# Optimization experiments

Measured on AMD Instinct MI355X. Metric: run time of the kernel, lower is better.

Reference implementation:

```python
import jax, jax.numpy as jnp
import numpy as np

N, M, P, H = 200000, 20, 64, 256
EPS = 1e-12  # inside sqrt: avoids NaN grads when duplicate neighbors give zero distance


def setup_inputs() -> dict:
    key = jax.random.key(0)
    ks = jax.random.split(key, 8)
    x = jax.random.normal(ks[0], (N, P), jnp.float32)
    pos = jax.random.uniform(ks[1], (N, 2), jnp.float32) * 10.0
    y = jax.random.normal(ks[2], (N,), jnp.float32)
    # m distinct-from-self neighbor indices per node (offset trick avoids self loops)
    off = jax.random.randint(ks[3], (N, M), 1, N)
    nbr_idx = ((jnp.arange(N)[:, None] + off) % N).astype(jnp.int32)
    theta = jnp.array([1.0, 1.0, 0.1], jnp.float32)  # (sigma_sq, phi, tau)
    w1 = jax.random.normal(ks[4], (P, H), jnp.float32) * (1.0 / np.sqrt(P))
    b1 = jnp.zeros((H,), jnp.float32)
    w2 = jax.random.normal(ks[5], (H, 1), jnp.float32) * (1.0 / np.sqrt(H))
    b2 = jnp.zeros((1,), jnp.float32)
    return dict(x=x, pos=pos, y=y, nbr_idx=nbr_idx, theta=theta,
                w1=w1, b1=b1, w2=w2, b2=b2)


def _dist(a, b):
    return jnp.sqrt(jnp.sum((a - b) ** 2, axis=-1) + EPS)


def reference(x, pos, y, nbr_idx, theta, w1, b1, w2, b2):
    sigma_sq, phi, tau = theta[0], theta[1], theta[2]
    tau_sq = tau * sigma_sq
    m = nbr_idx.shape[1]
    pos_nbr = pos[nbr_idx]                                            # [N,M,2] gather
    # Cov(i, N(i)): exponential covariance of node-to-neighbor distances  [N,M]
    cov_i_ni = sigma_sq * jnp.exp(-phi * _dist(pos[:, None, :], pos_nbr))
    # Cov(N(i), N(i)) + nugget on the diagonal                          [N,M,M]
    d_nn = _dist(pos_nbr[:, :, None, :], pos_nbr[:, None, :, :])
    cov = sigma_sq * jnp.exp(-phi * d_nn) + tau_sq * jnp.eye(m, dtype=pos.dtype)
    # B_i = Cov(N,N)^{-1} Cov(i,N)  (batched small solve == inv @ vec)  [N,M]
    b_i = jnp.linalg.solve(cov, cov_i_ni[..., None])[..., 0]
    f_i = sigma_sq + tau - jnp.sum(b_i * cov_i_ni, axis=1)             # [N]
    inv_sqrt_f = 1.0 / jnp.sqrt(f_i)
    # MLP: Linear -> ReLU -> Linear, squeezed to [N]
    o = (jax.nn.relu(x @ w1 + b1) @ w2 + b2)[:, 0]
    y_decor = (y - jnp.sum(y[nbr_idx] * b_i, axis=1)) * inv_sqrt_f
    o_decor = (o - jnp.sum(o[nbr_idx] * b_i, axis=1)) * inv_sqrt_f
    return (y_decor, o_decor, o)
```

## Files before the change

kernel.cpp:

```cpp
#include <hip/hip_runtime.h>


#define MM   20
#define PP   64
#define HH   256
#define EPSF 1e-12f
#define UT(r, c) ((r)*21 - ((r)*((r)-1))/2 + ((c)-(r)))

typedef __attribute__((ext_vector_type(8))) short bf16x8;
typedef __attribute__((ext_vector_type(4))) float f32x4;

static __device__ __forceinline__ unsigned short f2bf(float f) {
    unsigned int u = __builtin_bit_cast(unsigned int, f);
    u += 0x7fffu + ((u >> 16) & 1u);
    return (unsigned short)(u >> 16);
}
static __device__ __forceinline__ float bf2f(unsigned short h) {
    unsigned int u = ((unsigned int)h) << 16;
    return __builtin_bit_cast(float, u);
}

__global__ __launch_bounds__(256, 2)
void mlp_mfma_kernel(const float* __restrict__ x,
                     const float* __restrict__ w1,
                     const float* __restrict__ b1,
                     const float* __restrict__ w2,
                     const float* __restrict__ b2,
                     float* __restrict__ o_out, int n)
{
    __shared__ __align__(16) short swh[PP * HH];
    __shared__ __align__(16) short swl[PP * HH];
    const int tid = threadIdx.x;

    {
        const int col = tid;
        const int t = col >> 4, nn = col & 15;
        #pragma unroll
        for (int g = 0; g < 8; ++g) {
            const int s = g >> 2, q = g & 3;
            bf16x8 hv, lv;
            #pragma unroll
            for (int u = 0; u < 8; ++u) {
                float v = w1[(g * 8 + u) * HH + col];
                unsigned short h = f2bf(v);
                hv[u] = (short)h;
                lv[u] = (short)f2bf(v - bf2f(h));
            }
            const int base = ((((t * 2 + s) * 4 + q) * 16) + nn) * 8;
            *(bf16x8*)&swh[base] = hv;
            *(bf16x8*)&swl[base] = lv;
        }
    }
    __syncthreads();

    const int lane = tid & 63;
    const int wv   = tid >> 6;
    const int nn   = lane & 15;
    const int q    = lane >> 4;
    const int wb   = blockIdx.x * 256 + wv * 64;

    float w2v[16], b1v[16];
    #pragma unroll
    for (int t = 0; t < 16; ++t) {
        w2v[t] = w2[t * 16 + nn];
        b1v[t] = b1[t * 16 + nn];
    }

    bf16x8 ah[4][2], al[4][2];
    #pragma unroll
    for (int mt = 0; mt < 4; ++mt) {
        const int row = wb + mt * 16 + nn;
        #pragma unroll
        for (int s = 0; s < 2; ++s) {
            float v[8];
            if (row < n) {
                const float* xp = x + (size_t)row * PP + s * 32 + q * 8;
                float4 va = *(const float4*)(xp);
                float4 vb = *(const float4*)(xp + 4);
                v[0]=va.x; v[1]=va.y; v[2]=va.z; v[3]=va.w;
                v[4]=vb.x; v[5]=vb.y; v[6]=vb.z; v[7]=vb.w;
            } else {
                #pragma unroll
                for (int u = 0; u < 8; ++u) v[u] = 0.0f;
            }
            bf16x8 h, l;
            #pragma unroll
            for (int u = 0; u < 8; ++u) {
                unsigned short hb = f2bf(v[u]);
                h[u] = (short)hb;
                l[u] = (short)f2bf(v[u] - bf2f(hb));
            }
            ah[mt][s] = h;
            al[mt][s] = l;
        }
    }

    float part[4][4];
    #pragma unroll
    for (int mt = 0; mt < 4; ++mt)
        #pragma unroll
        for (int r = 0; r < 4; ++r) part[mt][r] = 0.0f;

    for (int t = 0; t < 16; ++t) {
        f32x4 acc[4];
        #pragma unroll
        for (int mt = 0; mt < 4; ++mt) acc[mt] = (f32x4)(0.0f);
        #pragma unroll
        for (int s = 0; s < 2; ++s) {
            const int fb = ((((t * 2 + s) * 4 + q) * 16) + nn) * 8;
            bf16x8 bh = *(const bf16x8*)&swh[fb];
            bf16x8 bl = *(const bf16x8*)&swl[fb];
            #pragma unroll
            for (int mt = 0; mt < 4; ++mt) {
                acc[mt] = __builtin_amdgcn_mfma_f32_16x16x32_bf16(ah[mt][s], bh, acc[mt], 0, 0, 0);
                acc[mt] = __builtin_amdgcn_mfma_f32_16x16x32_bf16(al[mt][s], bh, acc[mt], 0, 0, 0);
                acc[mt] = __builtin_amdgcn_mfma_f32_16x16x32_bf16(ah[mt][s], bl, acc[mt], 0, 0, 0);
            }
        }
        #pragma unroll
        for (int mt = 0; mt < 4; ++mt)
            #pragma unroll
            for (int r = 0; r < 4; ++r)
                part[mt][r] = fmaf(fmaxf(acc[mt][r] + b1v[t], 0.0f), w2v[t], part[mt][r]);
    }

    #pragma unroll
    for (int w = 1; w < 16; w <<= 1)
        #pragma unroll
        for (int mt = 0; mt < 4; ++mt)
            #pragma unroll
            for (int r = 0; r < 4; ++r)
                part[mt][r] += __shfl_xor(part[mt][r], w, 64);

    const float bb = b2[0];
    if (nn == 0) {
        #pragma unroll
        for (int mt = 0; mt < 4; ++mt) {
            const int row = wb + mt * 16 + q * 4;
            if (row < n) {
                float4 o4 = make_float4(part[mt][0] + bb, part[mt][1] + bb,
                                        part[mt][2] + bb, part[mt][3] + bb);
                *(float4*)&o_out[row] = o4;
            }
        }
    }
}

__global__ __launch_bounds__(64, 1)
void solve_kernel(const float* __restrict__ pos,
                  const float* __restrict__ y,
                  const int*   __restrict__ nbr,
                  const float* __restrict__ theta,
                  const float* __restrict__ o_in,
                  float* __restrict__ yd,
                  float* __restrict__ od, int n)
{
    const int i = blockIdx.x * 64 + threadIdx.x;
    if (i >= n) return;

    const float sigma_sq = theta[0];
    const float phi      = theta[1];
    const float tau      = theta[2];
    const float tau_sq   = tau * sigma_sq;

    const float L2E = 1.44269504088896340736f;
    const float c1  = -phi * L2E;
    const float c0  = __builtin_amdgcn_logf(sigma_sq);

    int idx[MM];
    const int4* nb4 = (const int4*)(nbr + (size_t)i * MM);
    #pragma unroll
    for (int k = 0; k < MM / 4; ++k) {
        int4 v = nb4[k];
        idx[4*k] = v.x; idx[4*k+1] = v.y; idx[4*k+2] = v.z; idx[4*k+3] = v.w;
    }

    float px[21], py[21];
    const float2* pos2 = (const float2*)pos;
    #pragma unroll
    for (int j = 0; j < MM; ++j) {
        float2 p = pos2[idx[j]];
        px[j] = p.x; py[j] = p.y;
    }
    {
        float2 p = pos2[i];
        px[20] = p.x; py[20] = p.y;
    }

    const float sqrtEPS = __builtin_amdgcn_sqrtf(EPSF);
    const float diagA   = __builtin_amdgcn_exp2f(fmaf(sqrtEPS, c1, c0)) + tau_sq;

    float a[231];
    #pragma unroll
    for (int r = 0; r < 21; ++r) {
        #pragma unroll
        for (int c = r; c < 21; ++c) {
            if (r == c) {
                a[UT(r, c)] = (r == 20) ? (sigma_sq + tau) : diagA;
            } else {
                float dx = px[r] - px[c];
                float dy = py[r] - py[c];
                float d2 = fmaf(dx, dx, fmaf(dy, dy, EPSF));
                float d  = __builtin_amdgcn_sqrtf(d2);
                a[UT(r, c)] = __builtin_amdgcn_exp2f(fmaf(d, c1, c0));
            }
        }
    }

    float yv[21], ov[21];
    #pragma unroll
    for (int j = 0; j < MM; ++j) {
        yv[j] = y[idx[j]];
        ov[j] = o_in[idx[j]];
    }
    yv[20] = y[i];
    ov[20] = o_in[i];

    float pr[21], pd, pyv, pov;
    #pragma unroll 1
    for (int k = 0; k < 20; ++k) {
        switch (k) {
#define CASE(K) case K: {                                     \
            pd = a[UT(K, K)]; pyv = yv[K]; pov = ov[K];       \
            _Pragma("unroll")                                 \
            for (int c = K; c < 21; ++c) pr[c] = a[UT(K, c)]; \
        } break;
        CASE(0)  CASE(1)  CASE(2)  CASE(3)  CASE(4)
        CASE(5)  CASE(6)  CASE(7)  CASE(8)  CASE(9)
        CASE(10) CASE(11) CASE(12) CASE(13) CASE(14)
        CASE(15) CASE(16) CASE(17) CASE(18) CASE(19)
#undef CASE
        default: break;
        }
        float rp = __builtin_amdgcn_rcpf(pd);
        rp = rp * (2.0f - pd * rp);
        float m[21];
        #pragma unroll
        for (int r = 0; r < 21; ++r) {
            float mr = pr[r] * rp;
            m[r] = (r > k) ? mr : 0.0f;
        }
        #pragma unroll
        for (int r = 0; r < 21; ++r) {
            #pragma unroll
            for (int c = r; c < 21; ++c)
                a[UT(r, c)] = fmaf(-m[r], pr[c], a[UT(r, c)]);
            yv[r] = fmaf(-m[r], pyv, yv[r]);
            ov[r] = fmaf(-m[r], pov, ov[r]);
        }
    }

    const float f = a[UT(20, 20)];
    float is = __builtin_amdgcn_rsqf(f);
    is = is * fmaf(-0.5f * f * is, is, 1.5f);
    yd[i] = yv[20] * is;
    od[i] = ov[20] * is;
}

extern "C" void kernel_launch(void* const* d_in, const int* in_sizes, int n_in,
                              void* d_out, int out_size, void* d_ws, size_t ws_size,
                              hipStream_t stream)
{
    const float* x     = (const float*)d_in[0];
    const float* pos   = (const float*)d_in[1];
    const float* y     = (const float*)d_in[2];
    const int*   nbr   = (const int*)  d_in[3];
    const float* theta = (const float*)d_in[4];
    const float* w1    = (const float*)d_in[5];
    const float* b1    = (const float*)d_in[6];
    const float* w2    = (const float*)d_in[7];
    const float* b2    = (const float*)d_in[8];

    const int n = in_sizes[2];
    float* out = (float*)d_out;
    float* yd = out;
    float* od = out + (size_t)n;
    float* oo = out + 2 * (size_t)n;

    mlp_mfma_kernel<<<(n + 255) / 256, 256, 0, stream>>>(x, w1, b1, w2, b2, oo, n);
    solve_kernel<<<(n + 63) / 64, 64, 0, stream>>>(pos, y, nbr, theta, oo, yd, od, n);
}
```

Baseline: 234.2 us.

## Split each node's Gaussian elimination across lane pairs with column-interleaved storage

The solve kernel now gives each node to two adjacent lanes. Each lane holds the even or odd columns of the upper-triangular matrix, and one lane carries the y right-hand side while the other carries the o right-hand side. Pivots and multipliers are swapped between the pair with shuffles. This roughly halves the per-thread register array and lets the elimination loop be fully unrolled instead of dispatching through a switch, which aims to cut register pressure and raise occupancy (launch bounds now allow 2 blocks). The cost is extra shuffles, duplicated distance work for the shared column, and twice as many threads. The MLP kernel's outer loop over t is also unrolled.

```diff
diff --git a/kernel.cpp b/kernel.cpp
--- a/kernel.cpp
+++ b/kernel.cpp
@@ -5,7 +5,10 @@
 #define PP   64
 #define HH   256
 #define EPSF 1e-12f
-#define UT(r, c) ((r)*21 - ((r)*((r)-1))/2 + ((c)-(r)))
+
+#define QH(r)     ((r) >> 1)
+#define AIDX(r)   (11*(r) - (QH(r)*(QH(r)-1) + ((r)&1)*QH(r)))
+#define AT(r, s)  aL[AIDX(r) + (s) - QH(r)]
 
 typedef __attribute__((ext_vector_type(8))) short bf16x8;
 typedef __attribute__((ext_vector_type(4))) float f32x4;
@@ -101,6 +104,7 @@
         #pragma unroll
         for (int r = 0; r < 4; ++r) part[mt][r] = 0.0f;
 
+    #pragma unroll
     for (int t = 0; t < 16; ++t) {
         f32x4 acc[4];
         #pragma unroll
@@ -146,7 +150,7 @@
     }
 }
 
-__global__ __launch_bounds__(64, 1)
+__global__ __launch_bounds__(64, 2)
 void solve_kernel(const float* __restrict__ pos,
                   const float* __restrict__ y,
                   const int*   __restrict__ nbr,
@@ -155,7 +159,9 @@
                   float* __restrict__ yd,
                   float* __restrict__ od, int n)
 {
-    const int i = blockIdx.x * 64 + threadIdx.x;
+    const int lane = threadIdx.x;
+    const int h_   = lane & 1;
+    const int i    = blockIdx.x * 32 + (lane >> 1);
     if (i >= n) return;
 
     const float sigma_sq = theta[0];
@@ -167,6 +173,10 @@
     const float c1  = -phi * L2E;
     const float c0  = __builtin_amdgcn_logf(sigma_sq);
 
+    const float sqrtEPS = __builtin_amdgcn_sqrtf(EPSF);
+    const float diagA   = __builtin_amdgcn_exp2f(fmaf(sqrtEPS, c1, c0)) + tau_sq;
+    const float diagB   = sigma_sq + tau;
+
     int idx[MM];
     const int4* nb4 = (const int4*)(nbr + (size_t)i * MM);
     #pragma unroll
@@ -187,74 +197,76 @@
         px[20] = p.x; py[20] = p.y;
     }
 
-    const float sqrtEPS = __builtin_amdgcn_sqrtf(EPSF);
-    const float diagA   = __builtin_amdgcn_exp2f(fmaf(sqrtEPS, c1, c0)) + tau_sq;
-
-    float a[231];
-    #pragma unroll
-    for (int r = 0; r < 21; ++r) {
-        #pragma unroll
-        for (int c = r; c < 21; ++c) {
-            if (r == c) {
-                a[UT(r, c)] = (r == 20) ? (sigma_sq + tau) : diagA;
-            } else {
-                float dx = px[r] - px[c];
-                float dy = py[r] - py[c];
-                float d2 = fmaf(dx, dx, fmaf(dy, dy, EPSF));
-                float d  = __builtin_amdgcn_sqrtf(d2);
-                a[UT(r, c)] = __builtin_amdgcn_exp2f(fmaf(d, c1, c0));
-            }
-        }
-    }
-
-    float yv[21], ov[21];
-    #pragma unroll
-    for (int j = 0; j < MM; ++j) {
-        yv[j] = y[idx[j]];
-        ov[j] = o_in[idx[j]];
-    }
-    yv[20] = y[i];
-    ov[20] = o_in[i];
-
-    float pr[21], pd, pyv, pov;
-    #pragma unroll 1
+    float pxc[11], pyc[11];
+    #pragma unroll
+    for (int s = 0; s < 10; ++s) {
+        pxc[s] = h_ ? px[2*s+1] : px[2*s];
+        pyc[s] = h_ ? py[2*s+1] : py[2*s];
+    }
+    pxc[10] = px[20];
+    pyc[10] = py[20];
+
+    float bv[21];
+    {
+        const float* src = h_ ? o_in : y;
+        #pragma unroll
+        for (int j = 0; j < MM; ++j) bv[j] = src[idx[j]];
+        bv[20] = src[i];
+    }
+
+    float aL[131];
+    #pragma unroll
+    for (int r = 0; r <= 20; ++r) {
+        #pragma unroll
+        for (int s = QH(r); s <= 10; ++s) {
+            float dx = px[r] - pxc[s];
+            float dy = py[r] - pyc[s];
+            float d  = __builtin_amdgcn_sqrtf(fmaf(dx, dx, fmaf(dy, dy, EPSF)));
+            float v  = __builtin_amdgcn_exp2f(fmaf(d, c1, c0));
+            if (s == QH(r)) {
+                const float dv = (r == 20) ? diagB : diagA;
+                v = (h_ == (r & 1)) ? dv : v;
+            }
+            AT(r, s) = v;
+        }
+    }
+
+    #pragma unroll
     for (int k = 0; k < 20; ++k) {
-        switch (k) {
-#define CASE(K) case K: {                                     \
-            pd = a[UT(K, K)]; pyv = yv[K]; pov = ov[K];       \
-            _Pragma("unroll")                                 \
-            for (int c = K; c < 21; ++c) pr[c] = a[UT(K, c)]; \
-        } break;
-        CASE(0)  CASE(1)  CASE(2)  CASE(3)  CASE(4)
-        CASE(5)  CASE(6)  CASE(7)  CASE(8)  CASE(9)
-        CASE(10) CASE(11) CASE(12) CASE(13) CASE(14)
-        CASE(15) CASE(16) CASE(17) CASE(18) CASE(19)
-#undef CASE
-        default: break;
-        }
+        float sendv = AT(k, QH(k));
+        float recvv = __shfl_xor(sendv, 1, 64);
+        float pd = ((k & 1) == h_) ? sendv : recvv;
         float rp = __builtin_amdgcn_rcpf(pd);
         rp = rp * (2.0f - pd * rp);
-        float m[21];
-        #pragma unroll
-        for (int r = 0; r < 21; ++r) {
-            float mr = pr[r] * rp;
-            m[r] = (r > k) ? mr : 0.0f;
-        }
-        #pragma unroll
-        for (int r = 0; r < 21; ++r) {
-            #pragma unroll
-            for (int c = r; c < 21; ++c)
-                a[UT(r, c)] = fmaf(-m[r], pr[c], a[UT(r, c)]);
-            yv[r] = fmaf(-m[r], pyv, yv[r]);
-            ov[r] = fmaf(-m[r], pov, ov[r]);
-        }
-    }
-
-    const float f = a[UT(20, 20)];
+
+        float ml[11], mo[11];
+        #pragma unroll
+        for (int s = QH(k); s <= 10; ++s) {
+            float v = AT(k, s) * rp;
+            if (s == QH(k))
+                v = (2*s + h_ > k) ? v : 0.0f;
+            ml[s] = v;
+            mo[s] = __shfl_xor(v, 1, 64);
+        }
+
+        #pragma unroll
+        for (int r = k + 1; r <= 20; ++r) {
+            float mr = ((r & 1) == h_) ? ml[QH(r)] : mo[QH(r)];
+            bv[r] = fmaf(-mr, bv[k], bv[r]);
+            #pragma unroll
+            for (int s = QH(r); s <= 10; ++s)
+                AT(r, s) = fmaf(-mr, AT(k, s), AT(r, s));
+        }
+    }
+
+    float fs = AT(20, 10);
+    float fo = __shfl_xor(fs, 1, 64);
+    float f  = h_ ? fo : fs;
     float is = __builtin_amdgcn_rsqf(f);
     is = is * fmaf(-0.5f * f * is, is, 1.5f);
-    yd[i] = yv[20] * is;
-    od[i] = ov[20] * is;
+
+    float* dst = h_ ? od : yd;
+    dst[i] = bv[20] * is;
 }
 
 extern "C" void kernel_launch(void* const* d_in, const int* in_sizes, int n_in,
@@ -278,5 +290,5 @@
     float* oo = out + 2 * (size_t)n;
 
     mlp_mfma_kernel<<<(n + 255) / 256, 256, 0, stream>>>(x, w1, b1, w2, b2, oo, n);
-    solve_kernel<<<(n + 63) / 64, 64, 0, stream>>>(pos, y, nbr, theta, oo, yd, od, n);
-}
+    solve_kernel<<<(n + 31) / 32, 64, 0, stream>>>(pos, y, nbr, theta, oo, yd, od, n);
+}
```

After: 697.1 us. 2.98x slower.
